# Kernel tuning notes

Hardware: AMD Instinct MI355X
Metric: run time of the kernel (lower is better)

## Reference

```python
import jax, jax.numpy as jnp
import numpy as np


def conv2d(x, w, b):
    # x: [B,C,H,W], w: [O,I,5,5], VALID, stride 1 (matches torch Conv2d defaults)
    y = jax.lax.conv_general_dilated(x, w, (1, 1), 'VALID',
                                     dimension_numbers=('NCHW', 'OIHW', 'NCHW'))
    return y + b[None, :, None, None]


def maxpool_2x5(x):
    # MaxPool2d(kernel=(2,5), stride=(2,1))
    return jax.lax.reduce_window(x, -jnp.inf, jax.lax.max,
                                 (1, 1, 2, 5), (1, 1, 2, 1), 'VALID')


def gru(x, w_ih, w_hh, b_ih, b_hh):
    # Faithful torch nn.GRU (batch_first=False): x is [L, N, 64]; gate order r,z,n.
    H = w_hh.shape[1]
    h0 = jnp.zeros((x.shape[1], H), x.dtype)

    def step(h, xt):
        gi = xt @ w_ih.T + b_ih
        gh = h @ w_hh.T + b_hh
        i_r, i_z, i_n = jnp.split(gi, 3, axis=-1)
        h_r, h_z, h_n = jnp.split(gh, 3, axis=-1)
        r = jax.nn.sigmoid(i_r + h_r)
        z = jax.nn.sigmoid(i_z + h_z)
        n = jnp.tanh(i_n + r * h_n)
        h_new = (1.0 - z) * n + z * h
        return h_new, h_new

    _, ys = jax.lax.scan(step, h0, x)
    return ys


def branch(x, w1, b1, w2, b2, w3, b3, lw, lb, gwih, gwhh, gbih, gbhh):
    x = x[:, None]                      # [B,1,H,W]
    x = conv2d(x, w1, b1)
    x = conv2d(x, w2, b2)
    x = conv2d(x, w3, b3)
    x = maxpool_2x5(x)                  # [B,64,58,W']
    B = x.shape[0]
    x = x.reshape(B, x.shape[-1], 3712)  # same row-major reshape as torch
    x = x @ lw.T + lb                   # [B,W',64]
    # nn.GRU without batch_first scans over dim 0 (batch!) — replicate exactly
    return gru(x, gwih, gwhh, gbih, gbhh)


def _make_params(key):
    ks = iter(jax.random.split(key, 40))
    def p(shape, scale=0.05):
        return (jax.random.normal(next(ks), shape, jnp.float32) * scale)
    d = {}
    for pre in ('e', 't'):
        d[f'{pre}_w1'] = p((16, 1, 5, 5)); d[f'{pre}_b1'] = p((16,))
        d[f'{pre}_w2'] = p((32, 16, 5, 5)); d[f'{pre}_b2'] = p((32,))
        d[f'{pre}_w3'] = p((64, 32, 5, 5)); d[f'{pre}_b3'] = p((64,))
        d[f'{pre}l_w'] = p((64, 3712), 0.01); d[f'{pre}l_b'] = p((64,))
        d[f'{pre}g_wih'] = p((192, 64)); d[f'{pre}g_whh'] = p((192, 64))
        d[f'{pre}g_bih'] = p((192,)); d[f'{pre}g_bhh'] = p((192,))
    d['a_w'] = p((1, 64)); d['a_b'] = p((1,))
    d['h_w'] = p((128, 64)); d['h_b'] = p((128,))
    d['c_w'] = p((2, 128)); d['c_b'] = p((2,))
    return d


def setup_inputs() -> dict:
    key = jax.random.key(0)
    k1, k2, k3 = jax.random.split(key, 3)
    inp = {
        'evaluation': jax.random.normal(k1, (4, 128, 2048), jnp.float32),
        'template': jax.random.normal(k2, (4, 128, 1040), jnp.float32),
    }
    inp.update(_make_params(k3))
    return inp


def reference(evaluation, template,
              e_w1, e_b1, e_w2, e_b2, e_w3, e_b3, el_w, el_b,
              eg_wih, eg_whh, eg_bih, eg_bhh,
              t_w1, t_b1, t_w2, t_b2, t_w3, t_b3, tl_w, tl_b,
              tg_wih, tg_whh, tg_bih, tg_bhh,
              a_w, a_b, h_w, h_b, c_w, c_b):
    e = branch(evaluation, e_w1, e_b1, e_w2, e_b2, e_w3, e_b3,
               el_w, el_b, eg_wih, eg_whh, eg_bih, eg_bhh)   # [B,Se,64]
    t = branch(template, t_w1, t_b1, t_w2, t_b2, t_w3, t_b3,
               tl_w, tl_b, tg_wih, tg_whh, tg_bih, tg_bhh)   # [B,St,64]
    # bmm(template, eval^T) -> [B,St,Se], softmax over Se
    tt = jax.nn.softmax(jnp.einsum('btd,bed->bte', t, e), axis=-1)
    # bmm(tt^T, template) -> [B,Se,64]
    tt = jnp.einsum('bte,btd->bed', tt, t)
    tt = jnp.abs(tt - e)
    # attention over eval sequence positions
    att = jax.nn.softmax((e @ a_w.T + a_b)[..., 0], axis=-1)  # [B,Se]
    # vectorized form of the original Python double loop
    red = jnp.einsum('bed,be->bd', tt, att)                   # [B,64]
    h = jax.nn.relu(red @ h_w.T + h_b)
    return jax.nn.softmax(h @ c_w.T + c_b, axis=-1)           # [B,2]
```

## Files before the change

### kernel.cpp

```cpp
#include <hip/hip_runtime.h>
#include <hip/hip_bf16.h>
#include <cmath>


typedef unsigned short u16;
typedef unsigned int u32;
typedef __attribute__((ext_vector_type(8))) short bf16x8;
typedef __attribute__((ext_vector_type(8))) unsigned short u16x8;
typedef __attribute__((ext_vector_type(16))) float f32x16;

__device__ __forceinline__ u16 f2bf(float f) {
  unsigned int x = __float_as_uint(f);
  return (u16)((x + 0x7fffu + ((x >> 16) & 1u)) >> 16);
}
__device__ __forceinline__ float bf2f(u16 v) {
  return __uint_as_float(((unsigned int)v) << 16);
}
__device__ __forceinline__ u32 f2bf_pk(float a, float b) {
  __hip_bfloat162 h = __float22bfloat162_rn(float2{a, b});
  u32 r;
  __builtin_memcpy(&r, &h, 4);
  return r;
}

static const size_t OFF_BEFF_E  = 0;
static const size_t OFF_BEFF_T  = 64;
static const size_t OFF_BIAS2_E = 128;
static const size_t OFF_BIAS2_T = 320;
static const size_t OFF_WKX_E   = 512;
static const size_t OFF_WKX_T   = 27136;
static const size_t OFF_W12P_E  = 53760;
static const size_t OFF_W12P_T  = 63008;
static const size_t OFF_B12_E   = 72256;
static const size_t OFF_B12_T   = 72288;
static const size_t OFF_LWT1_E  = 72320;
static const size_t OFF_LWT1_T  = 191104;
static const size_t OFF_ATT     = 309888;
static const size_t OFF_XYBF_E  = 318016;
static const size_t OFF_XYBF_T  = 578112;
static const size_t OFF_TTBF    = 709184;
static const size_t OFF_LIN_E   = 840256;
static const size_t OFF_LIN_T   = 1360448;
static const size_t OFF_PV      = 1622592;
static const size_t OFF_RED     = 2142784;
static const size_t OFF_RSUM    = 2143040;
static const size_t ZERO_F4     = 326720;
static const size_t ZSTRIDE     = 617;
static const size_t OFF_GI_E    = 2147136;
static const size_t OFF_GI_T    = 3707712;
static const size_t OFF_P       = 4494144;

__global__ __launch_bounds__(320) void prep_kernel(
    const float* __restrict__ w1e, const float* __restrict__ b1e,
    const float* __restrict__ w2e, const float* __restrict__ b2e,
    const float* __restrict__ w1t, const float* __restrict__ b1t,
    const float* __restrict__ w2t, const float* __restrict__ b2t,
    float* __restrict__ w12p_e, float* __restrict__ w12p_t,
    float* __restrict__ b12o_e, float* __restrict__ b12o_t,
    const float* __restrict__ wih_e, const float* __restrict__ bih_e,
    const float* __restrict__ lb_e, float* __restrict__ bias2_e,
    const float* __restrict__ wih_t, const float* __restrict__ bih_t,
    const float* __restrict__ lb_t, float* __restrict__ bias2_t,
    const float* __restrict__ lwe, const float* __restrict__ lwt,
    u16* __restrict__ lwt1_e, u16* __restrict__ lwt1_t,
    float4* __restrict__ zbase) {
  const int bx = blockIdx.x;
  const int tid = threadIdx.x;
  {
    const size_t base = (size_t)bx * ZSTRIDE;
    const float4 z = {0.f, 0.f, 0.f, 0.f};
    for (size_t i = base + tid; i < base + ZSTRIDE && i < ZERO_F4; i += 320)
      zbase[i] = z;
  }
  if (bx >= 66) {
    if (tid < 256) {
      const int k = bx - 66;
      const int br = k / 232, j = k - br * 232;
      const float* src = br ? lwt : lwe;
      u16* dst = br ? lwt1_t : lwt1_e;
      const int e = j * 1024 + tid * 4;
      const int h = e >> 12;
      const int rem = e & 4095;
      const int n = rem >> 6, c = rem & 63;
      const float* s = src + (size_t)n * 3712 + (size_t)c * 58 + h;
      const float v0 = s[0], v1 = s[58], v2 = s[116], v3 = s[174];
      *(u32*)&dst[e] = f2bf_pk(v0, v1);
      *(u32*)&dst[e + 2] = f2bf_pk(v2, v3);
    }
    return;
  }
  if (bx >= 64) {
    const int br = bx - 64;
    const float* wih = br ? wih_t : wih_e;
    const float* bih = br ? bih_t : bih_e;
    const float* lb = br ? lb_t : lb_e;
    float* bias2 = br ? bias2_t : bias2_e;
    __shared__ float s_lb[64];
    if (tid < 64) s_lb[tid] = lb[tid];
    __syncthreads();
    if (tid < 192) {
      float acc = bih[tid];
      const float* wr = wih + tid * 64;
      for (int d = 0; d < 64; ++d) acc = fmaf(wr[d], s_lb[d], acc);
      bias2[tid] = acc;
    }
    return;
  }
  const int br = bx >> 5;
  const float* w1 = br ? w1t : w1e;
  const float* b1 = br ? b1t : b1e;
  const float* w2 = br ? w2t : w2e;
  const float* b2 = br ? b2t : b2e;
  float* w12p = br ? w12p_t : w12p_e;
  float* b12o = br ? b12o_t : b12o_e;
  const int c12 = bx & 31;
  __shared__ float s_w1pad[16 * 169];
  __shared__ float s_w2c[400];
  __shared__ float s_b1[16];
  for (int i = tid; i < 2704; i += 320) s_w1pad[i] = 0.f;
  if (tid < 16) s_b1[tid] = b1[tid];
  __syncthreads();
  for (int i = tid; i < 400; i += 320) {
    const int c1 = i / 25, r = (i % 25) / 5, cc = i % 5;
    s_w1pad[c1 * 169 + (r + 4) * 13 + (cc + 4)] = w1[i];
    s_w2c[i] = w2[c12 * 400 + i];
  }
  __syncthreads();
  if (tid < 289) {
    const int py = tid / 17, px = tid % 17;
    float v = 0.f;
    if (py >= 4 && py <= 12 && px >= 4 && px <= 12) {
      const int sy = py - 4, sx = px - 4;
      float accs[2] = {0.f, 0.f};
      for (int c1 = 0; c1 < 16; ++c1) {
        const float* w2p = s_w2c + c1 * 25;
        const float* w1p = s_w1pad + c1 * 169 + (sy + 4) * 13 + (sx + 4);
#pragma unroll
        for (int uy = 0; uy < 5; ++uy)
#pragma unroll
          for (int ux = 0; ux < 5; ++ux)
            accs[uy & 1] = fmaf(w2p[uy * 5 + ux], w1p[-(uy * 13) - ux], accs[uy & 1]);
      }
      v = accs[0] + accs[1];
    }
    w12p[c12 * 289 + tid] = v;
  } else if (tid == 300) {
    float acc = b2[c12];
    for (int c1 = 0; c1 < 16; ++c1) {
      float sw = 0.f;
      for (int u = 0; u < 25; ++u) sw += s_w2c[c1 * 25 + u];
      acc = fmaf(sw, s_b1[c1], acc);
    }
    b12o[c12] = acc;
  }
}

__global__ __launch_bounds__(256) void compose_weff_kernel(
    const float* __restrict__ w3e, const float* __restrict__ b3e,
    const float* __restrict__ w3t, const float* __restrict__ b3t,
    const float* __restrict__ w12p_e, const float* __restrict__ w12p_t,
    const float* __restrict__ b12_e, const float* __restrict__ b12_t,
    u16* __restrict__ wkx_e, u16* __restrict__ wkx_t,
    float* __restrict__ beff_e, float* __restrict__ beff_t) {
  const int br = blockIdx.y;
  const float* w3 = br ? w3t : w3e;
  const float* b3 = br ? b3t : b3e;
  const float* w12p = br ? w12p_t : w12p_e;
  const float* b12 = br ? b12_t : b12_e;
  u16* wkx = br ? wkx_t : wkx_e;
  float* beff = br ? beff_t : beff_e;
  const int o = blockIdx.x;
  __shared__ float s_pad[32 * 289];
  __shared__ float s_w3o[800];
  __shared__ float s_b12[32];
  const int tid = threadIdx.x;
  for (int i = tid; i < 9248; i += 256) s_pad[i] = w12p[i];
  for (int i = tid; i < 800; i += 256) s_w3o[i] = w3[o * 800 + i];
  if (tid < 32) s_b12[tid] = b12[tid];
  __syncthreads();
  if (tid < 169) {
    const int sy = tid / 13, sx = tid % 13;
    float accs[4] = {0.f, 0.f, 0.f, 0.f};
#pragma unroll 4
    for (int c = 0; c < 32; ++c) {
      const float* w3p = s_w3o + c * 25;
      const float* wp = s_pad + c * 289 + (sy + 4) * 17 + (sx + 4);
#pragma unroll
      for (int uy = 0; uy < 5; ++uy)
#pragma unroll
        for (int ux = 0; ux < 5; ++ux)
          accs[c & 3] = fmaf(w3p[uy * 5 + ux], wp[-(uy * 17) - ux], accs[c & 3]);
    }
    const u16 v = f2bf(accs[0] + accs[1] + accs[2] + accs[3]);
#pragma unroll
    for (int p = 0; p < 4; ++p)
      wkx[((p * 13 + sx) * 64 + o) * 16 + sy + p] = v;
  } else if (tid < 169 + 156) {
    const int t = tid - 169, kx = t / 12, q = t % 12;
    const int p = q / 3, idx = q % 3;
    const int slot = (idx < p) ? idx : (p + 13) + (idx - p);
    wkx[((p * 13 + kx) * 64 + o) * 16 + slot] = 0;
  }
  if (tid == 255) {
    float acc = b3[o];
    for (int c = 0; c < 32; ++c) {
      float sw = 0.f;
      for (int u = 0; u < 25; ++u) sw += s_w3o[c * 25 + u];
      acc = fmaf(sw, s_b12[c], acc);
    }
    beff[o] = acc;
  }
}

__global__ __launch_bounds__(256, 2) void conv_pool_lin_kernel(
    const float* __restrict__ xe, const u16* __restrict__ wkx_e,
    const float* __restrict__ beff_e, const u16* __restrict__ lwt1_e,
    float* __restrict__ lin_e,
    const float* __restrict__ xt, const u16* __restrict__ wkx_t,
    const float* __restrict__ beff_t, const u16* __restrict__ lwt1_t,
    float* __restrict__ lin_t) {
  const int zz = blockIdx.z;
  const bool ev = zz < 4;
  const int b = ev ? zz : zz - 4;
  const int W = ev ? 2048 : 1040;
  const int T = ev ? 2032 : 1024;
  const int cb = blockIdx.x * 60;
  if (cb >= T) return;
  const float* x = ev ? xe : xt;
  const u16* wkx = ev ? wkx_e : wkx_t;
  const float* beff = ev ? beff_e : beff_t;
  const u16* lwt1 = ev ? lwt1_e : lwt1_t;
  float* lin = ev ? lin_e : lin_t;

  __shared__ __align__(16) u16 s_x[80 * 24];
  __shared__ __align__(16) u16 s_out[2 * 64 * 72];
  __shared__ __align__(16) u16 s_poolT[64 * 72];
  __shared__ float s_beff[64];

  const int tid = threadIdx.x;
  const int lane = tid & 63, wave = tid >> 6;
  const int rsel = wave & 1, cm = (wave >> 1) * 32;
  const int l31 = lane & 31, g8 = (lane >> 5) * 8;
  const int th = (wave & 1) * 32, nh = (wave >> 1) * 32;

  if (tid < 64) s_beff[tid] = beff[tid];

  const int by0 = blockIdx.y * 3;
  const int by1 = (by0 + 3 < 29) ? (by0 + 3) : 29;

  const int pr_ = tid < 384 ? ((tid & 127) + (tid >> 7) * 128) : 0;
  (void)pr_;
  float p0[3], p1[3];
  {
    const float* xb = x + ((size_t)b * 128 + 4 * by0) * W;
#pragma unroll
    for (int k = 0; k < 3; ++k) {
      const int i = tid + k * 256;
      if (i < 640) {
        const int pr = i / 80, c = i - pr * 80;
        int gc = cb + c;
        if (gc > W - 1) gc = W - 1;
        p0[k] = xb[(size_t)(2 * pr) * W + gc];
        p1[k] = xb[(size_t)(2 * pr + 1) * W + gc];
      }
    }
  }

  f32x16 accL = {};
  for (int by = by0; by < by1; ++by) {
#pragma unroll
    for (int k = 0; k < 3; ++k) {
      const int i = tid + k * 256;
      if (i < 640) {
        const int pr = i / 80, c = i - pr * 80;
        *(u32*)&s_x[c * 24 + 2 * pr] = f2bf_pk(p0[k], p1[k]);
      }
    }
    if (by + 1 < by1) {
      const float* xb = x + ((size_t)b * 128 + 4 * (by + 1)) * W;
#pragma unroll
      for (int k = 0; k < 3; ++k) {
        const int i = tid + k * 256;
        if (i < 640) {
          const int pr = i / 80, c = i - pr * 80;
          int gc = cb + c;
          if (gc > W - 1) gc = W - 1;
          p0[k] = xb[(size_t)(2 * pr) * W + gc];
          p1[k] = xb[(size_t)(2 * pr + 1) * W + gc];
        }
      }
    }
    __syncthreads();
#pragma unroll
    for (int hh = 0; hh < 2; ++hh) {
      const int p = 2 * hh + rsel;
      const int h = 2 * by + hh;
      bf16x8 wfrag[13];
      {
        const u16* aw = wkx + ((p * 13) * 64 + cm + l31) * 16 + g8;
#pragma unroll
        for (int kx = 0; kx < 13; ++kx) wfrag[kx] = *(const bf16x8*)(aw + kx * 1024);
      }
      bf16x8 bb[4];
      {
        const u16* bp2 = lwt1 + ((size_t)(h * 64 + nh + l31)) * 64 + g8;
#pragma unroll
        for (int ks = 0; ks < 4; ++ks) bb[ks] = *(const bf16x8*)(bp2 + ks * 16);
      }
      f32x16 c0a = {}, c1a = {}, c0b = {}, c1b = {};
      const u16* bxp = s_x + g8;
#pragma unroll
      for (int kx = 0; kx < 6; ++kx) {
        bf16x8 b0 = *(const bf16x8*)(bxp + (l31 + kx) * 24);
        bf16x8 b1 = *(const bf16x8*)(bxp + (32 + l31 + kx) * 24);
        bf16x8 b0q = *(const bf16x8*)(bxp + (l31 + kx + 7) * 24);
        bf16x8 b1q = *(const bf16x8*)(bxp + (32 + l31 + kx + 7) * 24);
        c0a = __builtin_amdgcn_mfma_f32_32x32x16_bf16(wfrag[kx], b0, c0a, 0, 0, 0);
        c1a = __builtin_amdgcn_mfma_f32_32x32x16_bf16(wfrag[kx], b1, c1a, 0, 0, 0);
        c0b = __builtin_amdgcn_mfma_f32_32x32x16_bf16(wfrag[kx + 7], b0q, c0b, 0, 0, 0);
        c1b = __builtin_amdgcn_mfma_f32_32x32x16_bf16(wfrag[kx + 7], b1q, c1b, 0, 0, 0);
      }
      {
        bf16x8 b0 = *(const bf16x8*)(bxp + (l31 + 6) * 24);
        bf16x8 b1 = *(const bf16x8*)(bxp + (32 + l31 + 6) * 24);
        c0a = __builtin_amdgcn_mfma_f32_32x32x16_bf16(wfrag[6], b0, c0a, 0, 0, 0);
        c1a = __builtin_amdgcn_mfma_f32_32x32x16_bf16(wfrag[6], b1, c1a, 0, 0, 0);
      }
#pragma unroll
      for (int r = 0; r < 16; ++r) {
        const int c = cm + (r & 3) + 8 * (r >> 2) + (g8 >> 1);
        u16* o = s_out + (rsel * 64 + c) * 72;
        const u32 pk = f2bf_pk(c0a[r] + c0b[r], c1a[r] + c1b[r]);
        o[l31] = (u16)pk;
        o[32 + l31] = (u16)(pk >> 16);
      }
      __syncthreads();
      {
        const int pc = tid & 63, tg = tid >> 6;
        const int t0 = tg * 16;
        const float bias = s_beff[pc];
        const u16* r0p = s_out + pc * 72 + t0;
        const u16* r1p = s_out + (64 + pc) * 72 + t0;
        const u16x8 a0 = *(const u16x8*)(r0p);
        const u16x8 a1 = *(const u16x8*)(r0p + 8);
        const u16x8 a2 = *(const u16x8*)(r0p + 16);
        const u16x8 q0 = *(const u16x8*)(r1p);
        const u16x8 q1 = *(const u16x8*)(r1p + 8);
        const u16x8 q2 = *(const u16x8*)(r1p + 16);
        float m01[20];
#pragma unroll
        for (int j = 0; j < 8; ++j) {
          m01[j] = fmaxf(bf2f(a0[j]), bf2f(q0[j]));
          m01[j + 8] = fmaxf(bf2f(a1[j]), bf2f(q1[j]));
          if (j < 4) m01[j + 16] = fmaxf(bf2f(a2[j]), bf2f(q2[j]));
        }
#pragma unroll
        for (int i = 0; i < 16; ++i) {
          if (t0 + i < 60) {
            float m = m01[i];
#pragma unroll
            for (int k = 1; k < 5; ++k) m = fmaxf(m, m01[i + k]);
            s_poolT[(t0 + i) * 72 + pc] = f2bf(m + bias);
          }
        }
      }
      __syncthreads();
      {
        const u16* ap2 = s_poolT + (th + l31) * 72 + g8;
#pragma unroll
        for (int ks = 0; ks < 4; ++ks) {
          bf16x8 a = *(const bf16x8*)(ap2 + ks * 16);
          accL = __builtin_amdgcn_mfma_f32_32x32x16_bf16(a, bb[ks], accL, 0, 0, 0);
        }
      }
    }
  }
  {
    const int nn = nh + l31;
#pragma unroll
    for (int r = 0; r < 16; ++r) {
      const int t = th + (r & 3) + 8 * (r >> 2) + (g8 >> 1);
      const int tt = cb + t;
      if (t < 60 && tt < T)
        atomicAdd(&lin[((size_t)b * T + tt) * 64 + nn], accL[r]);
    }
  }
}

__global__ __launch_bounds__(256) void gemm_gi_kernel(
    const float* __restrict__ Ae, const float* __restrict__ Wte,
    const float* __restrict__ biase, float* __restrict__ oute,
    const float* __restrict__ At, const float* __restrict__ Wtt,
    const float* __restrict__ biast, float* __restrict__ outt) {
  const int bx = blockIdx.x;
  const bool ev = bx < 127;
  const float* A = ev ? Ae : At;
  const float* Wt = ev ? Wte : Wtt;
  const float* bias = ev ? biase : biast;
  float* out = ev ? oute : outt;
  const int r0 = (ev ? bx : bx - 127) * 64;
  const int N = 192, K = 64;
  __shared__ float sA[64 * 33];
  __shared__ float sB[64 * 33];
  const int tid = threadIdx.x;
  const int n0 = blockIdx.y * 64;
  const int ty = tid >> 4, tx = tid & 15;
  float acc[4][4] = {};
  for (int kc = 0; kc < K; kc += 32) {
    __syncthreads();
#pragma unroll
    for (int rep = 0; rep < 8; ++rep) {
      const int l = tid + rep * 256;
      const int row = l >> 5, kk = l & 31;
      sA[row * 33 + kk] = A[(size_t)(r0 + row) * K + kc + kk];
      sB[row * 33 + kk] = Wt[(size_t)(n0 + row) * K + kc + kk];
    }
    __syncthreads();
#pragma unroll 8
    for (int kk = 0; kk < 32; ++kk) {
      const float a0 = sA[(ty * 4 + 0) * 33 + kk];
      const float a1 = sA[(ty * 4 + 1) * 33 + kk];
      const float a2 = sA[(ty * 4 + 2) * 33 + kk];
      const float a3 = sA[(ty * 4 + 3) * 33 + kk];
      const float b0 = sB[(tx * 4 + 0) * 33 + kk];
      const float b1 = sB[(tx * 4 + 1) * 33 + kk];
      const float b2 = sB[(tx * 4 + 2) * 33 + kk];
      const float b3 = sB[(tx * 4 + 3) * 33 + kk];
      acc[0][0] = fmaf(a0, b0, acc[0][0]); acc[0][1] = fmaf(a0, b1, acc[0][1]);
      acc[0][2] = fmaf(a0, b2, acc[0][2]); acc[0][3] = fmaf(a0, b3, acc[0][3]);
      acc[1][0] = fmaf(a1, b0, acc[1][0]); acc[1][1] = fmaf(a1, b1, acc[1][1]);
      acc[1][2] = fmaf(a1, b2, acc[1][2]); acc[1][3] = fmaf(a1, b3, acc[1][3]);
      acc[2][0] = fmaf(a2, b0, acc[2][0]); acc[2][1] = fmaf(a2, b1, acc[2][1]);
      acc[2][2] = fmaf(a2, b2, acc[2][2]); acc[2][3] = fmaf(a2, b3, acc[2][3]);
      acc[3][0] = fmaf(a3, b0, acc[3][0]); acc[3][1] = fmaf(a3, b1, acc[3][1]);
      acc[3][2] = fmaf(a3, b2, acc[3][2]); acc[3][3] = fmaf(a3, b3, acc[3][3]);
    }
  }
#pragma unroll
  for (int i = 0; i < 4; ++i)
#pragma unroll
    for (int j = 0; j < 4; ++j)
      out[(size_t)(r0 + ty * 4 + i) * N + n0 + tx * 4 + j] =
          acc[i][j] + bias[n0 + tx * 4 + j];
}

__global__ __launch_bounds__(256) void gru_rec_kernel(
    float* __restrict__ xyE, const float* __restrict__ giE,
    const float* __restrict__ whhE, const float* __restrict__ bhhE,
    float* __restrict__ xyT, const float* __restrict__ giT,
    const float* __restrict__ whhT, const float* __restrict__ bhhT,
    u16* __restrict__ xybfE, u16* __restrict__ xybfT, u16* __restrict__ ttbf,
    const float* __restrict__ a_w, const float* __restrict__ a_b,
    float* __restrict__ logits) {
  const int bxid = blockIdx.x;
  const bool ev = bxid < 127;
  float* xy = ev ? xyE : xyT;
  u16* xybf = ev ? xybfE : xybfT;
  const float* gi = ev ? giE : giT;
  const float* whh = ev ? whhE : whhT;
  const float* bhh = ev ? bhhE : bhhT;
  const int T = ev ? 2032 : 1024;
  const int t0 = (ev ? bxid : bxid - 127) * 16;
  __shared__ float s_whh_t[64 * 192];
  __shared__ float s_h[16][64];
  __shared__ float s_aw[64];
  const int tid = threadIdx.x;
  const int lane = tid & 63, wave = tid >> 6;
  for (int i = tid; i < 192 * 64; i += 256) {
    const int j = i >> 6, d = i & 63;
    s_whh_t[d * 192 + j] = whh[i];
  }
  for (int i = tid; i < 16 * 64; i += 256) (&s_h[0][0])[i] = 0.f;
  if (tid < 64) s_aw[tid] = a_w[tid];
  const float ab = a_b[0];
  const float bhr = bhh[lane], bhz = bhh[64 + lane], bhn = bhh[128 + lane];
  __syncthreads();
  for (int b = 0; b < 4; ++b) {
    float gir[4], giz[4], gin[4];
#pragma unroll
    for (int sl = 0; sl < 4; ++sl) {
      int t = t0 + wave * 4 + sl; if (t > T - 1) t = T - 1;
      const float* girow = gi + ((size_t)b * T + t) * 192;
      gir[sl] = girow[lane]; giz[sl] = girow[64 + lane]; gin[sl] = girow[128 + lane];
    }
    float ahr[4] = {}, ahz[4] = {}, ahn[4] = {};
    for (int d = 0; d < 64; ++d) {
      const float wr_ = s_whh_t[d * 192 + lane];
      const float wz_ = s_whh_t[d * 192 + 64 + lane];
      const float wn_ = s_whh_t[d * 192 + 128 + lane];
#pragma unroll
      for (int sl = 0; sl < 4; ++sl) {
        const float hv = s_h[wave * 4 + sl][d];
        ahr[sl] = fmaf(wr_, hv, ahr[sl]);
        ahz[sl] = fmaf(wz_, hv, ahz[sl]);
        ahn[sl] = fmaf(wn_, hv, ahn[sl]);
      }
    }
    float hn[4];
#pragma unroll
    for (int sl = 0; sl < 4; ++sl) {
      const float r = 1.f / (1.f + __expf(-(gir[sl] + ahr[sl] + bhr)));
      const float z = 1.f / (1.f + __expf(-(giz[sl] + ahz[sl] + bhz)));
      const float n = tanhf(gin[sl] + r * (ahn[sl] + bhn));
      hn[sl] = (1.f - z) * n + z * s_h[wave * 4 + sl][lane];
    }
    __syncthreads();
#pragma unroll
    for (int sl = 0; sl < 4; ++sl) {
      const int t = t0 + wave * 4 + sl;
      s_h[wave * 4 + sl][lane] = hn[sl];
      if (t < T) {
        const size_t idx = ((size_t)b * T + t) * 64 + lane;
        xy[idx] = hn[sl];
        xybf[idx] = f2bf(hn[sl]);
        if (ev) {
          float v = hn[sl] * s_aw[lane];
#pragma unroll
          for (int off = 32; off > 0; off >>= 1) v += __shfl_down(v, off, 64);
          if (lane == 0) logits[b * 2032 + t] = v + ab;
        } else {
          ttbf[((size_t)b * 64 + lane) * 1024 + t] = f2bf(hn[sl]);
        }
      }
    }
    __syncthreads();
  }
}

__global__ __launch_bounds__(256) void scores_mfma_kernel(
    const u16* __restrict__ tbf, const u16* __restrict__ ebf,
    u16* __restrict__ P, float* __restrict__ rowsum) {
  __shared__ __align__(16) u16 sA[64 * 72];
  __shared__ __align__(16) u16 sB[128 * 72];
  const int tid = threadIdx.x;
  const int b = blockIdx.z;
  const int tau0 = blockIdx.x * 64;
  const int e0 = blockIdx.y * 128;
  const int lane = tid & 63, wave = tid >> 6;
  const int l31 = lane & 31, g8 = (lane >> 5) * 8;
  {
    const int row = tid >> 2, seg = (tid & 3) * 16;
    const u16* ap = &tbf[((size_t)b * 1024 + tau0 + row) * 64 + seg];
    u16* da = &sA[row * 72 + seg];
    *(u16x8*)da = *(const u16x8*)ap;
    *(u16x8*)(da + 8) = *(const u16x8*)(ap + 8);
  }
#pragma unroll
  for (int r = 0; r < 4; ++r) {
    const int q = tid + r * 256;
    const int row = q >> 3, seg = (q & 7) * 8;
    int eps = e0 + row; if (eps > 2031) eps = 2031;
    *(u16x8*)&sB[row * 72 + seg] =
        *(const u16x8*)&ebf[((size_t)b * 2032 + eps) * 64 + seg];
  }
  __syncthreads();
  const int mh = (wave & 1) * 32;
  const int nq = (wave >> 1) * 64;
  f32x16 acc0 = {}, acc1 = {};
#pragma unroll
  for (int ks = 0; ks < 4; ++ks) {
    bf16x8 a = *(const bf16x8*)&sA[(mh + l31) * 72 + ks * 16 + g8];
    bf16x8 b0 = *(const bf16x8*)&sB[(nq + l31) * 72 + ks * 16 + g8];
    bf16x8 b1 = *(const bf16x8*)&sB[(nq + 32 + l31) * 72 + ks * 16 + g8];
    acc0 = __builtin_amdgcn_mfma_f32_32x32x16_bf16(a, b0, acc0, 0, 0, 0);
    acc1 = __builtin_amdgcn_mfma_f32_32x32x16_bf16(a, b1, acc1, 0, 0, 0);
  }
  const int ep0 = e0 + nq + l31;
  const int ep1 = ep0 + 32;
#pragma unroll
  for (int r = 0; r < 16; ++r) {
    const int tau = tau0 + mh + (r & 3) + 8 * (r >> 2) + (g8 >> 1);
    const size_t prow = ((size_t)b * 1024 + tau) * 2032;
    const float e0v = __expf(acc0[r]);
    const float e1v = __expf(acc1[r]);
    float part = 0.f;
    if (ep0 < 2032) { P[prow + ep0] = f2bf(e0v); part += e0v; }
    if (ep1 < 2032) { P[prow + ep1] = f2bf(e1v); part += e1v; }
#pragma unroll
    for (int off = 16; off > 0; off >>= 1) part += __shfl_down(part, off, 32);
    if (l31 == 0) atomicAdd(&rowsum[b * 1024 + tau], part);
  }
}

__global__ __launch_bounds__(256) void pv_mfma_kernel(
    const u16* __restrict__ P, const u16* __restrict__ ttbf,
    const float* __restrict__ rowsum, float* __restrict__ PV) {
  __shared__ __align__(16) u16 sPT[64 * 72];
  __shared__ __align__(16) u16 sTT[64 * 72];
  const int tid = threadIdx.x;
  const int b = blockIdx.z;
  const int e0 = blockIdx.x * 64;
  const int tau_base = blockIdx.y * 256;
  const int lane = tid & 63, wave = tid >> 6;
  const int l31 = lane & 31, g8 = (lane >> 5) * 8;
  const int mh = (wave & 1) * 32, nh = (wave >> 1) * 32;
  f32x16 acc = {};
  for (int cc = 0; cc < 4; ++cc) {
    const int tc = tau_base + cc * 64;
    __syncthreads();
#pragma unroll
    for (int k = 0; k < 2; ++k) {
      const int q = tid + k * 256;
      const int row = q >> 3, seg = (q & 7) * 8;
      const float inv = 1.0f / rowsum[b * 1024 + tc + row];
      int er = e0 + seg;
      if (er > 2032 - 8) er = 2032 - 8;
      const u16x8 v = *(const u16x8*)&P[((size_t)b * 1024 + tc + row) * 2032 + er];
#pragma unroll
      for (int j = 0; j < 8; ++j)
        sPT[(seg + j) * 72 + row] = f2bf(bf2f(v[j]) * inv);
    }
#pragma unroll
    for (int k = 0; k < 2; ++k) {
      const int q = tid + k * 256;
      const int row = q >> 3, seg = (q & 7) * 8;
      *(u16x8*)&sTT[row * 72 + seg] =
          *(const u16x8*)&ttbf[((size_t)b * 64 + row) * 1024 + tc + seg];
    }
    __syncthreads();
#pragma unroll
    for (int ks = 0; ks < 4; ++ks) {
      bf16x8 a = *(const bf16x8*)&sPT[(mh + l31) * 72 + ks * 16 + g8];
      bf16x8 bb = *(const bf16x8*)&sTT[(nh + l31) * 72 + ks * 16 + g8];
      acc = __builtin_amdgcn_mfma_f32_32x32x16_bf16(a, bb, acc, 0, 0, 0);
    }
  }
#pragma unroll
  for (int r = 0; r < 16; ++r) {
    const int eps = e0 + mh + (r & 3) + 8 * (r >> 2) + (g8 >> 1);
    if (eps < 2032)
      atomicAdd(&PV[((size_t)b * 2032 + eps) * 64 + nh + l31], acc[r]);
  }
}

__global__ __launch_bounds__(256) void red_reduce_kernel(
    const float* __restrict__ emat, const float* __restrict__ PV,
    const float* __restrict__ logits, float* __restrict__ red) {
  __shared__ float s_att[2032];
  __shared__ float sred[4];
  __shared__ float s_part[4][64];
  const int tid = threadIdx.x;
  const int lane = tid & 63, wave = tid >> 6;
  const int b = blockIdx.y;
  float m = -3.4e38f;
  for (int i = tid; i < 2032; i += 256) {
    const float v = logits[b * 2032 + i];
    s_att[i] = v;
    m = fmaxf(m, v);
  }
#pragma unroll
  for (int off = 32; off > 0; off >>= 1) m = fmaxf(m, __shfl_down(m, off, 64));
  if (lane == 0) sred[wave] = m;
  __syncthreads();
  m = fmaxf(fmaxf(sred[0], sred[1]), fmaxf(sred[2], sred[3]));
  __syncthreads();
  float ssum = 0.f;
  for (int i = tid; i < 2032; i += 256) {
    const float v = __expf(s_att[i] - m);
    s_att[i] = v;
    ssum += v;
  }
#pragma unroll
  for (int off = 32; off > 0; off >>= 1) ssum += __shfl_down(ssum, off, 64);
  if (lane == 0) sred[wave] = ssum;
  __syncthreads();
  const float inv = 1.f / (sred[0] + sred[1] + sred[2] + sred[3]);
  const int i0 = blockIdx.x * 127;
  float acc = 0.f;
  for (int i = i0 + wave; i < i0 + 127; i += 4) {
    const size_t idx = ((size_t)b * 2032 + i) * 64 + lane;
    acc = fmaf(fabsf(PV[idx] - emat[idx]), s_att[i], acc);
  }
  s_part[wave][lane] = acc;
  __syncthreads();
  if (tid < 64)
    atomicAdd(&red[b * 64 + tid],
              (s_part[0][tid] + s_part[1][tid] + s_part[2][tid] + s_part[3][tid]) * inv);
}

__global__ __launch_bounds__(128) void mlp_kernel(
    const float* __restrict__ red, const float* __restrict__ h_w,
    const float* __restrict__ h_b, const float* __restrict__ c_w,
    const float* __restrict__ c_b, float* __restrict__ out) {
  __shared__ float s_red[64];
  __shared__ float s_hv[128];
  const int tid = threadIdx.x;
  const int b = blockIdx.x;
  if (tid < 64) s_red[tid] = red[b * 64 + tid];
  __syncthreads();
  {
    float acc = h_b[tid];
    const float* hw = h_w + tid * 64;
    for (int d = 0; d < 64; ++d) acc = fmaf(s_red[d], hw[d], acc);
    s_hv[tid] = fmaxf(acc, 0.f);
  }
  __syncthreads();
  if (tid == 0) {
    float l0 = c_b[0], l1 = c_b[1];
    for (int j = 0; j < 128; ++j) {
      l0 = fmaf(s_hv[j], c_w[j], l0);
      l1 = fmaf(s_hv[j], c_w[128 + j], l1);
    }
    const float mm = fmaxf(l0, l1);
    const float e0 = __expf(l0 - mm), e1 = __expf(l1 - mm);
    const float invs = 1.f / (e0 + e1);
    out[b * 2 + 0] = e0 * invs;
    out[b * 2 + 1] = e1 * invs;
  }
}

extern "C" void kernel_launch(void* const* d_in, const int* in_sizes, int n_in,
                              void* d_out, int out_size, void* d_ws, size_t ws_size,
                              hipStream_t stream) {
  const float* evaluation = (const float*)d_in[0];
  const float* templ      = (const float*)d_in[1];
  const float* e_w1 = (const float*)d_in[2];
  const float* e_b1 = (const float*)d_in[3];
  const float* e_w2 = (const float*)d_in[4];
  const float* e_b2 = (const float*)d_in[5];
  const float* e_w3 = (const float*)d_in[6];
  const float* e_b3 = (const float*)d_in[7];
  const float* el_w = (const float*)d_in[8];
  const float* el_b = (const float*)d_in[9];
  const float* eg_wih = (const float*)d_in[10];
  const float* eg_whh = (const float*)d_in[11];
  const float* eg_bih = (const float*)d_in[12];
  const float* eg_bhh = (const float*)d_in[13];
  const float* t_w1 = (const float*)d_in[14];
  const float* t_b1 = (const float*)d_in[15];
  const float* t_w2 = (const float*)d_in[16];
  const float* t_b2 = (const float*)d_in[17];
  const float* t_w3 = (const float*)d_in[18];
  const float* t_b3 = (const float*)d_in[19];
  const float* tl_w = (const float*)d_in[20];
  const float* tl_b = (const float*)d_in[21];
  const float* tg_wih = (const float*)d_in[22];
  const float* tg_whh = (const float*)d_in[23];
  const float* tg_bih = (const float*)d_in[24];
  const float* tg_bhh = (const float*)d_in[25];
  const float* a_w = (const float*)d_in[26];
  const float* a_b = (const float*)d_in[27];
  const float* h_w = (const float*)d_in[28];
  const float* h_b = (const float*)d_in[29];
  const float* c_w = (const float*)d_in[30];
  const float* c_b = (const float*)d_in[31];

  float* ws = (float*)d_ws;
  float* beff_e  = ws + OFF_BEFF_E;
  float* beff_t  = ws + OFF_BEFF_T;
  float* bias2_e = ws + OFF_BIAS2_E;
  float* bias2_t = ws + OFF_BIAS2_T;
  u16*   wkx_e   = (u16*)(ws + OFF_WKX_E);
  u16*   wkx_t   = (u16*)(ws + OFF_WKX_T);
  float* w12p_e  = ws + OFF_W12P_E;
  float* w12p_t  = ws + OFF_W12P_T;
  float* b12_e   = ws + OFF_B12_E;
  float* b12_t   = ws + OFF_B12_T;
  u16*   lwt1_e  = (u16*)(ws + OFF_LWT1_E);
  u16*   lwt1_t  = (u16*)(ws + OFF_LWT1_T);
  float* attbuf  = ws + OFF_ATT;
  u16*   xybf_e  = (u16*)(ws + OFF_XYBF_E);
  u16*   xybf_t  = (u16*)(ws + OFF_XYBF_T);
  u16*   ttbf    = (u16*)(ws + OFF_TTBF);
  float* lin_e   = ws + OFF_LIN_E;
  float* lin_t   = ws + OFF_LIN_T;
  float* PVbuf   = ws + OFF_PV;
  float* redbuf  = ws + OFF_RED;
  float* rsum    = ws + OFF_RSUM;
  float* gi_e    = ws + OFF_GI_E;
  float* gi_t    = ws + OFF_GI_T;
  u16*   Pbuf    = (u16*)(ws + OFF_P);

  prep_kernel<<<530, 320, 0, stream>>>(
      e_w1, e_b1, e_w2, e_b2, t_w1, t_b1, t_w2, t_b2, w12p_e, w12p_t, b12_e, b12_t,
      eg_wih, eg_bih, el_b, bias2_e, tg_wih, tg_bih, tl_b, bias2_t,
      el_w, tl_w, lwt1_e, lwt1_t, (float4*)lin_e);
  compose_weff_kernel<<<dim3(64, 2), 256, 0, stream>>>(
      e_w3, e_b3, t_w3, t_b3, w12p_e, w12p_t, b12_e, b12_t, wkx_e, wkx_t, beff_e, beff_t);

  conv_pool_lin_kernel<<<dim3(34, 10, 8), 256, 0, stream>>>(
      evaluation, wkx_e, beff_e, lwt1_e, lin_e,
      templ, wkx_t, beff_t, lwt1_t, lin_t);
  gemm_gi_kernel<<<dim3(191, 3), 256, 0, stream>>>(
      lin_e, eg_wih, bias2_e, gi_e, lin_t, tg_wih, bias2_t, gi_t);
  gru_rec_kernel<<<191, 256, 0, stream>>>(
      lin_e, gi_e, eg_whh, eg_bhh, lin_t, gi_t, tg_whh, tg_bhh,
      xybf_e, xybf_t, ttbf, a_w, a_b, attbuf);

  scores_mfma_kernel<<<dim3(16, 16, 4), 256, 0, stream>>>(xybf_t, xybf_e, Pbuf, rsum);
  pv_mfma_kernel<<<dim3(32, 4, 4), 256, 0, stream>>>(Pbuf, ttbf, rsum, PVbuf);

  red_reduce_kernel<<<dim3(16, 4), 256, 0, stream>>>(lin_e, PVbuf, attbuf, redbuf);
  mlp_kernel<<<4, 128, 0, stream>>>(redbuf, h_w, h_b, c_w, c_b, (float*)d_out);
}
```

Baseline: 305.9 us.

## Recompute attention scores in PV kernel instead of materializing P matrix

```diff
diff --git a/kernel.cpp b/kernel.cpp
--- a/kernel.cpp
+++ b/kernel.cpp
@@ -41,14 +41,13 @@
 static const size_t OFF_TTBF    = 709184;
 static const size_t OFF_LIN_E   = 840256;
 static const size_t OFF_LIN_T   = 1360448;
-static const size_t OFF_PV      = 1622592;
-static const size_t OFF_RED     = 2142784;
-static const size_t OFF_RSUM    = 2143040;
-static const size_t ZERO_F4     = 326720;
-static const size_t ZSTRIDE     = 617;
+static const size_t OFF_RED     = 1622592;
+static const size_t OFF_RSUM    = 1622848;
+static const size_t ZERO_F4     = 196672;
+static const size_t ZSTRIDE     = 372;
+static const size_t OFF_ATTW    = 1626944;
 static const size_t OFF_GI_E    = 2147136;
 static const size_t OFF_GI_T    = 3707712;
-static const size_t OFF_P       = 4494144;
 
 __global__ __launch_bounds__(320) void prep_kernel(
     const float* __restrict__ w1e, const float* __restrict__ b1e,
@@ -248,8 +247,6 @@
   const int by0 = blockIdx.y * 3;
   const int by1 = (by0 + 3 < 29) ? (by0 + 3) : 29;
 
-  const int pr_ = tid < 384 ? ((tid & 127) + (tid >> 7) * 128) : 0;
-  (void)pr_;
   float p0[3], p1[3];
   {
     const float* xb = x + ((size_t)b * 128 + 4 * by0) * W;
@@ -527,9 +524,9 @@
   }
 }
 
-__global__ __launch_bounds__(256) void scores_mfma_kernel(
+__global__ __launch_bounds__(256) void rowsum_kernel(
     const u16* __restrict__ tbf, const u16* __restrict__ ebf,
-    u16* __restrict__ P, float* __restrict__ rowsum) {
+    float* __restrict__ rowsum) {
   __shared__ __align__(16) u16 sA[64 * 72];
   __shared__ __align__(16) u16 sB[128 * 72];
   const int tid = threadIdx.x;
@@ -570,45 +567,89 @@
 #pragma unroll
   for (int r = 0; r < 16; ++r) {
     const int tau = tau0 + mh + (r & 3) + 8 * (r >> 2) + (g8 >> 1);
-    const size_t prow = ((size_t)b * 1024 + tau) * 2032;
-    const float e0v = __expf(acc0[r]);
-    const float e1v = __expf(acc1[r]);
     float part = 0.f;
-    if (ep0 < 2032) { P[prow + ep0] = f2bf(e0v); part += e0v; }
-    if (ep1 < 2032) { P[prow + ep1] = f2bf(e1v); part += e1v; }
+    if (ep0 < 2032) part += __expf(acc0[r]);
+    if (ep1 < 2032) part += __expf(acc1[r]);
 #pragma unroll
     for (int off = 16; off > 0; off >>= 1) part += __shfl_down(part, off, 32);
     if (l31 == 0) atomicAdd(&rowsum[b * 1024 + tau], part);
   }
 }
 
-__global__ __launch_bounds__(256) void pv_mfma_kernel(
-    const u16* __restrict__ P, const u16* __restrict__ ttbf,
-    const float* __restrict__ rowsum, float* __restrict__ PV) {
+__global__ __launch_bounds__(256) void att_softmax_kernel(
+    const float* __restrict__ logits, float* __restrict__ attw) {
+  __shared__ float s_att[2032];
+  __shared__ float sred[4];
+  const int tid = threadIdx.x;
+  const int lane = tid & 63, wave = tid >> 6;
+  const int b = blockIdx.x;
+  float m = -3.4e38f;
+  for (int i = tid; i < 2032; i += 256) {
+    const float v = logits[b * 2032 + i];
+    s_att[i] = v;
+    m = fmaxf(m, v);
+  }
+#pragma unroll
+  for (int off = 32; off > 0; off >>= 1) m = fmaxf(m, __shfl_down(m, off, 64));
+  if (lane == 0) sred[wave] = m;
+  __syncthreads();
+  m = fmaxf(fmaxf(sred[0], sred[1]), fmaxf(sred[2], sred[3]));
+  __syncthreads();
+  float ssum = 0.f;
+  for (int i = tid; i < 2032; i += 256) {
+    const float v = __expf(s_att[i] - m);
+    s_att[i] = v;
+    ssum += v;
+  }
+#pragma unroll
+  for (int off = 32; off > 0; off >>= 1) ssum += __shfl_down(ssum, off, 64);
+  if (lane == 0) sred[wave] = ssum;
+  __syncthreads();
+  const float inv = 1.f / (sred[0] + sred[1] + sred[2] + sred[3]);
+  for (int i = tid; i < 2032; i += 256) attw[b * 2032 + i] = s_att[i] * inv;
+}
+
+__global__ __launch_bounds__(256) void pv_red_kernel(
+    const u16* __restrict__ tbf, const u16* __restrict__ ebf,
+    const u16* __restrict__ ttbf, const float* __restrict__ rowsum,
+    const float* __restrict__ attw, const float* __restrict__ emat,
+    float* __restrict__ red) {
+  __shared__ __align__(16) u16 sE[64 * 72];
+  __shared__ __align__(16) u16 sT[64 * 72];
+  __shared__ __align__(16) u16 sTT[64 * 72];
   __shared__ __align__(16) u16 sPT[64 * 72];
-  __shared__ __align__(16) u16 sTT[64 * 72];
+  __shared__ float s_rs[64];
+  __shared__ float s_att[64];
+  __shared__ float s_part[4][32];
   const int tid = threadIdx.x;
-  const int b = blockIdx.z;
+  const int b = blockIdx.y;
   const int e0 = blockIdx.x * 64;
-  const int tau_base = blockIdx.y * 256;
   const int lane = tid & 63, wave = tid >> 6;
   const int l31 = lane & 31, g8 = (lane >> 5) * 8;
-  const int mh = (wave & 1) * 32, nh = (wave >> 1) * 32;
-  f32x16 acc = {};
-  for (int cc = 0; cc < 4; ++cc) {
-    const int tc = tau_base + cc * 64;
+  const int mh = (wave & 1) * 32;
+  const int nh = (wave >> 1) * 32;
+  {
+    const int row = tid >> 2, seg = (tid & 3) * 16;
+    int eps = e0 + row; if (eps > 2031) eps = 2031;
+    const u16* ap = &ebf[((size_t)b * 2032 + eps) * 64 + seg];
+    u16* da = &sE[row * 72 + seg];
+    *(u16x8*)da = *(const u16x8*)ap;
+    *(u16x8*)(da + 8) = *(const u16x8*)(ap + 8);
+  }
+  if (tid < 64) {
+    const int e = e0 + tid;
+    s_att[tid] = (e < 2032) ? attw[b * 2032 + e] : 0.f;
+  }
+  f32x16 accPV = {};
+  for (int ch = 0; ch < 16; ++ch) {
+    const int tc = ch * 64;
     __syncthreads();
-#pragma unroll
-    for (int k = 0; k < 2; ++k) {
-      const int q = tid + k * 256;
-      const int row = q >> 3, seg = (q & 7) * 8;
-      const float inv = 1.0f / rowsum[b * 1024 + tc + row];
-      int er = e0 + seg;
-      if (er > 2032 - 8) er = 2032 - 8;
-      const u16x8 v = *(const u16x8*)&P[((size_t)b * 1024 + tc + row) * 2032 + er];
-#pragma unroll
-      for (int j = 0; j < 8; ++j)
-        sPT[(seg + j) * 72 + row] = f2bf(bf2f(v[j]) * inv);
+    {
+      const int row = tid >> 2, seg = (tid & 3) * 16;
+      const u16* ap = &tbf[((size_t)b * 1024 + tc + row) * 64 + seg];
+      u16* da = &sT[row * 72 + seg];
+      *(u16x8*)da = *(const u16x8*)ap;
+      *(u16x8*)(da + 8) = *(const u16x8*)(ap + 8);
     }
 #pragma unroll
     for (int k = 0; k < 2; ++k) {
@@ -617,65 +658,48 @@
       *(u16x8*)&sTT[row * 72 + seg] =
           *(const u16x8*)&ttbf[((size_t)b * 64 + row) * 1024 + tc + seg];
     }
+    if (tid < 64) s_rs[tid] = 1.0f / rowsum[b * 1024 + tc + tid];
+    __syncthreads();
+    f32x16 acc = {};
+#pragma unroll
+    for (int ks = 0; ks < 4; ++ks) {
+      bf16x8 a = *(const bf16x8*)&sT[(mh + l31) * 72 + ks * 16 + g8];
+      bf16x8 bb = *(const bf16x8*)&sE[(nh + l31) * 72 + ks * 16 + g8];
+      acc = __builtin_amdgcn_mfma_f32_32x32x16_bf16(a, bb, acc, 0, 0, 0);
+    }
+#pragma unroll
+    for (int r = 0; r < 16; ++r) {
+      const int tl = mh + (r & 3) + 8 * (r >> 2) + (g8 >> 1);
+      const int el = nh + l31;
+      sPT[el * 72 + tl] = f2bf(__expf(acc[r]) * s_rs[tl]);
+    }
     __syncthreads();
 #pragma unroll
     for (int ks = 0; ks < 4; ++ks) {
       bf16x8 a = *(const bf16x8*)&sPT[(mh + l31) * 72 + ks * 16 + g8];
       bf16x8 bb = *(const bf16x8*)&sTT[(nh + l31) * 72 + ks * 16 + g8];
-      acc = __builtin_amdgcn_mfma_f32_32x32x16_bf16(a, bb, acc, 0, 0, 0);
-    }
-  }
+      accPV = __builtin_amdgcn_mfma_f32_32x32x16_bf16(a, bb, accPV, 0, 0, 0);
+    }
+  }
+  float local = 0.f;
 #pragma unroll
   for (int r = 0; r < 16; ++r) {
-    const int eps = e0 + mh + (r & 3) + 8 * (r >> 2) + (g8 >> 1);
-    if (eps < 2032)
-      atomicAdd(&PV[((size_t)b * 2032 + eps) * 64 + nh + l31], acc[r]);
-  }
-}
-
-__global__ __launch_bounds__(256) void red_reduce_kernel(
-    const float* __restrict__ emat, const float* __restrict__ PV,
-    const float* __restrict__ logits, float* __restrict__ red) {
-  __shared__ float s_att[2032];
-  __shared__ float sred[4];
-  __shared__ float s_part[4][64];
-  const int tid = threadIdx.x;
-  const int lane = tid & 63, wave = tid >> 6;
-  const int b = blockIdx.y;
-  float m = -3.4e38f;
-  for (int i = tid; i < 2032; i += 256) {
-    const float v = logits[b * 2032 + i];
-    s_att[i] = v;
-    m = fmaxf(m, v);
-  }
-#pragma unroll
-  for (int off = 32; off > 0; off >>= 1) m = fmaxf(m, __shfl_down(m, off, 64));
-  if (lane == 0) sred[wave] = m;
-  __syncthreads();
-  m = fmaxf(fmaxf(sred[0], sred[1]), fmaxf(sred[2], sred[3]));
-  __syncthreads();
-  float ssum = 0.f;
-  for (int i = tid; i < 2032; i += 256) {
-    const float v = __expf(s_att[i] - m);
-    s_att[i] = v;
-    ssum += v;
-  }
-#pragma unroll
-  for (int off = 32; off > 0; off >>= 1) ssum += __shfl_down(ssum, off, 64);
-  if (lane == 0) sred[wave] = ssum;
-  __syncthreads();
-  const float inv = 1.f / (sred[0] + sred[1] + sred[2] + sred[3]);
-  const int i0 = blockIdx.x * 127;
-  float acc = 0.f;
-  for (int i = i0 + wave; i < i0 + 127; i += 4) {
-    const size_t idx = ((size_t)b * 2032 + i) * 64 + lane;
-    acc = fmaf(fabsf(PV[idx] - emat[idx]), s_att[i], acc);
-  }
-  s_part[wave][lane] = acc;
-  __syncthreads();
-  if (tid < 64)
-    atomicAdd(&red[b * 64 + tid],
-              (s_part[0][tid] + s_part[1][tid] + s_part[2][tid] + s_part[3][tid]) * inv);
+    const int el = mh + (r & 3) + 8 * (r >> 2) + (g8 >> 1);
+    const int eps = e0 + el;
+    if (eps < 2032) {
+      const size_t idx = ((size_t)b * 2032 + eps) * 64 + nh + l31;
+      local = fmaf(fabsf(accPV[r] - emat[idx]), s_att[el], local);
+    }
+  }
+  local += __shfl_xor(local, 32, 64);
+  if (lane < 32) s_part[wave][lane] = local;
+  __syncthreads();
+  if (tid < 64) {
+    const int d = tid;
+    const float v = (d < 32) ? (s_part[0][d] + s_part[1][d])
+                             : (s_part[2][d - 32] + s_part[3][d - 32]);
+    atomicAdd(&red[b * 64 + d], v);
+  }
 }
 
 __global__ __launch_bounds__(128) void mlp_kernel(
@@ -764,12 +788,11 @@
   u16*   ttbf    = (u16*)(ws + OFF_TTBF);
   float* lin_e   = ws + OFF_LIN_E;
   float* lin_t   = ws + OFF_LIN_T;
-  float* PVbuf   = ws + OFF_PV;
   float* redbuf  = ws + OFF_RED;
   float* rsum    = ws + OFF_RSUM;
+  float* attw    = ws + OFF_ATTW;
   float* gi_e    = ws + OFF_GI_E;
   float* gi_t    = ws + OFF_GI_T;
-  u16*   Pbuf    = (u16*)(ws + OFF_P);
 
   prep_kernel<<<530, 320, 0, stream>>>(
       e_w1, e_b1, e_w2, e_b2, t_w1, t_b1, t_w2, t_b2, w12p_e, w12p_t, b12_e, b12_t,
@@ -787,9 +810,10 @@
       lin_e, gi_e, eg_whh, eg_bhh, lin_t, gi_t, tg_whh, tg_bhh,
       xybf_e, xybf_t, ttbf, a_w, a_b, attbuf);
 
-  scores_mfma_kernel<<<dim3(16, 16, 4), 256, 0, stream>>>(xybf_t, xybf_e, Pbuf, rsum);
-  pv_mfma_kernel<<<dim3(32, 4, 4), 256, 0, stream>>>(Pbuf, ttbf, rsum, PVbuf);
-
-  red_reduce_kernel<<<dim3(16, 4), 256, 0, stream>>>(lin_e, PVbuf, attbuf, redbuf);
+  rowsum_kernel<<<dim3(16, 16, 4), 256, 0, stream>>>(xybf_t, xybf_e, rsum);
+  att_softmax_kernel<<<4, 256, 0, stream>>>(attbuf, attw);
+  pv_red_kernel<<<dim3(32, 4), 256, 0, stream>>>(
+      xybf_t, xybf_e, ttbf, rsum, attw, lin_e, redbuf);
+
   mlp_kernel<<<4, 128, 0, stream>>>(redbuf, h_w, h_b, c_w, c_b, (float*)d_out);
 }
```

After: 307.2 us (median of 2 runs). About the same (+0.4%).
